# Kernel tuning notes

Hardware: AMD Instinct MI355X
Metric: run time of the kernel (lower is better)

The kernel has to match this reference:

```python
import jax, jax.numpy as jnp
import numpy as np

B, S, D, H, FF = 2, 2048, 1024, 16, 4096
DH = D // H
EPS = 1e-5


def rmsnorm(x, g):
    rms = jnp.sqrt(jnp.mean(x * x, axis=-1, keepdims=True) + EPS)
    return x / rms * g


def gelu(x):
    return x * 0.5 * (1.0 + jax.lax.erf(x / np.float32(np.sqrt(2.0))))


def setup_inputs() -> dict:
    key = jax.random.key(0)
    ks = jax.random.split(key, 9)
    sd = np.float32(1.0 / np.sqrt(D))
    sf = np.float32(1.0 / np.sqrt(FF))
    return {
        'x': jax.random.normal(ks[0], (B, S, D), jnp.float32),
        'wq': jax.random.normal(ks[1], (D, D), jnp.float32) * sd,
        'wk': jax.random.normal(ks[2], (D, D), jnp.float32) * sd,
        'wv': jax.random.normal(ks[3], (D, D), jnp.float32) * sd,
        'wo': jax.random.normal(ks[4], (D, D), jnp.float32) * sd,
        'w1': jax.random.normal(ks[5], (FF, D), jnp.float32) * sd,
        'w2': jax.random.normal(ks[6], (D, FF), jnp.float32) * sf,
        'g1': jax.random.uniform(ks[7], (D,), jnp.float32),
        'g2': jax.random.uniform(ks[8], (D,), jnp.float32),
    }


def reference(x, wq, wk, wv, wo, w1, w2, g1, g2):
    b, s, d = x.shape
    h = rmsnorm(x, g1)
    # torch Linear: y = x @ W.T ; split heads -> [b, s, H, DH]
    q = jnp.einsum('bsd,ed->bse', h, wq).reshape(b, s, H, DH)
    k = jnp.einsum('bsd,ed->bse', h, wk).reshape(b, s, H, DH)
    v = jnp.einsum('bsd,ed->bse', h, wv).reshape(b, s, H, DH)
    score = jnp.einsum('bqhd,bkhd->bhqk', q, k) / np.float32(np.sqrt(DH))
    causal = jnp.triu(jnp.ones((s, s), bool), 1)  # strictly upper = masked
    score = score + jnp.where(causal, jnp.float32(-1e9), jnp.float32(0.0))
    attn_w = jax.nn.softmax(score, axis=-1)
    o = jnp.einsum('bhqk,bkhd->bqhd', attn_w, v).reshape(b, s, d)
    attn_out = jnp.einsum('bsd,ed->bse', o, wo)
    x2 = attn_out + x
    h2 = rmsnorm(x2, g2)
    ffn = jnp.einsum('bsf,df->bsd', gelu(jnp.einsum('bsd,fd->bsf', h2, w1)), w2)
    return ffn + x2
```

## Files before the change

### kernel.cpp

```cpp
#include <hip/hip_runtime.h>
#include <cstdint>

#define B_ 2
#define S_ 2048
#define D_ 1024
#define H_ 16
#define DH_ 64
#define FF_ 4096
#define M_TOK (B_ * S_)

typedef __attribute__((ext_vector_type(8))) short short8;
typedef __attribute__((ext_vector_type(4))) float f32x4;
typedef __attribute__((ext_vector_type(4))) unsigned short us4;

typedef unsigned short u16;

#define SCL 0.18033688011112042f

__device__ __forceinline__ float bf2f(u16 u) {
  union { uint32_t u; float f; } x;
  x.u = ((uint32_t)u) << 16;
  return x.f;
}
__device__ __forceinline__ u16 f2bf(float f) {
  union { float f; uint32_t u; } x;
  x.f = f;
  uint32_t r = x.u + 0x7FFFu + ((x.u >> 16) & 1u);
  return (u16)(r >> 16);
}

__device__ __forceinline__ void gl_lds16(const void* g, void* l) {
  __builtin_amdgcn_global_load_lds(
      (const __attribute__((address_space(1))) uint32_t*)(uintptr_t)g,
      (__attribute__((address_space(3))) uint32_t*)(uintptr_t)l, 16, 0, 0);
}

__device__ __forceinline__ float gelu_f(float v) {
  const float y = 0.7978845608f * (v + 0.044715f * v * v * v);
  const float t = exp2f(y * 2.885390082f);
  const float th = 1.0f - 2.0f * __builtin_amdgcn_rcpf(t + 1.0f);
  return 0.5f * v * (1.0f + th);
}

#define MEG 1048576
__global__ __launch_bounds__(256) void cvt_all_k(const float* __restrict__ wq, const float* __restrict__ wk,
                                                 const float* __restrict__ wv, const float* __restrict__ wo,
                                                 const float* __restrict__ w1, const float* __restrict__ w2,
                                                 u16* __restrict__ wqkv, u16* __restrict__ wob,
                                                 u16* __restrict__ w1b, u16* __restrict__ w2b) {
  const int n = (blockIdx.x * 256 + threadIdx.x) * 4;
  const float* src;
  u16* dst;
  int off;
  if (n < 3 * MEG) {
    dst = wqkv; off = n;
    src = (n < MEG) ? wq + n : (n < 2 * MEG ? wk + (n - MEG) : wv + (n - 2 * MEG));
  } else if (n < 4 * MEG) {
    dst = wob; off = n - 3 * MEG; src = wo + off;
  } else if (n < 8 * MEG) {
    dst = w1b; off = n - 4 * MEG; src = w1 + off;
  } else {
    dst = w2b; off = n - 8 * MEG; src = w2 + off;
  }
  const float4 v = *(const float4*)src;
  us4 o;
  o[0] = f2bf(v.x); o[1] = f2bf(v.y); o[2] = f2bf(v.z); o[3] = f2bf(v.w);
  *(us4*)&dst[off] = o;
}

__global__ __launch_bounds__(256) void zero_k(float* __restrict__ Of, float* __restrict__ L) {
  const int i = (blockIdx.x * 256 + threadIdx.x) * 4;
  if (i < 4 * MEG) { *(float4*)&Of[i] = float4{0.f, 0.f, 0.f, 0.f}; }
  else { *(float4*)&L[i - 4 * MEG] = float4{0.f, 0.f, 0.f, 0.f}; }
}

__global__ __launch_bounds__(256) void norm_o_k(const float* __restrict__ Of, const float* __restrict__ L,
                                                u16* __restrict__ O) {
  const int row = blockIdx.x;
  const int tid = threadIdx.x;
  const int col = tid * 4;
  const int hh = col >> 6;
  const float lv = L[(size_t)((row >> 11) * 16 + hh) * 2048 + (row & 2047)];
  const float inv = 1.0f / lv;
  const float4 v = *(const float4*)&Of[(size_t)row * D_ + col];
  us4 o;
  o[0] = f2bf(v.x * inv); o[1] = f2bf(v.y * inv);
  o[2] = f2bf(v.z * inv); o[3] = f2bf(v.w * inv);
  *(us4*)&O[(size_t)row * D_ + col] = o;
}

__global__ __launch_bounds__(256) void rmsnorm_k(const float* __restrict__ X,
                                                 const float* __restrict__ G,
                                                 u16* __restrict__ Hout) {
  const int row = blockIdx.x;
  const int tid = threadIdx.x;
  const float4 xx = *(const float4*)&X[(size_t)row * D_ + tid * 4];
  float v[4] = {xx.x, xx.y, xx.z, xx.w};
  float s = 0.f;
#pragma unroll
  for (int i = 0; i < 4; ++i) s += v[i] * v[i];
#pragma unroll
  for (int d = 1; d < 64; d <<= 1) s += __shfl_xor(s, d);
  __shared__ float red[4];
  if ((tid & 63) == 0) red[tid >> 6] = s;
  __syncthreads();
  s = red[0] + red[1] + red[2] + red[3];
  const float scale = rsqrtf(s * (1.0f / (float)D_) + 1e-5f);
  const float4 gg = *(const float4*)&G[tid * 4];
  us4 o;
  o[0] = f2bf(v[0] * scale * gg.x);
  o[1] = f2bf(v[1] * scale * gg.y);
  o[2] = f2bf(v[2] * scale * gg.z);
  o[3] = f2bf(v[3] * scale * gg.w);
  *(us4*)&Hout[(size_t)row * D_ + tid * 4] = o;
}

__global__ __launch_bounds__(256) void rmsnorm_wo_k(const u16* __restrict__ P0, const u16* __restrict__ P1,
                                                    const float* __restrict__ X, const float* __restrict__ G,
                                                    float* __restrict__ X2, u16* __restrict__ Hout) {
  const int row = blockIdx.x;
  const int tid = threadIdx.x;
  const size_t off = (size_t)row * D_ + tid * 4;
  const us4 p0 = *(const us4*)&P0[off];
  const us4 p1 = *(const us4*)&P1[off];
  const float4 xx = *(const float4*)&X[off];
  float v[4];
  v[0] = bf2f(p0[0]) + bf2f(p1[0]) + xx.x;
  v[1] = bf2f(p0[1]) + bf2f(p1[1]) + xx.y;
  v[2] = bf2f(p0[2]) + bf2f(p1[2]) + xx.z;
  v[3] = bf2f(p0[3]) + bf2f(p1[3]) + xx.w;
  *(float4*)&X2[off] = float4{v[0], v[1], v[2], v[3]};
  float s = 0.f;
#pragma unroll
  for (int i = 0; i < 4; ++i) s += v[i] * v[i];
#pragma unroll
  for (int d = 1; d < 64; d <<= 1) s += __shfl_xor(s, d);
  __shared__ float red[4];
  if ((tid & 63) == 0) red[tid >> 6] = s;
  __syncthreads();
  s = red[0] + red[1] + red[2] + red[3];
  const float scale = rsqrtf(s * (1.0f / (float)D_) + 1e-5f);
  const float4 gg = *(const float4*)&G[tid * 4];
  us4 o;
  o[0] = f2bf(v[0] * scale * gg.x);
  o[1] = f2bf(v[1] * scale * gg.y);
  o[2] = f2bf(v[2] * scale * gg.z);
  o[3] = f2bf(v[3] * scale * gg.w);
  *(us4*)&Hout[off] = o;
}

__global__ __launch_bounds__(256) void ffn2_red_k(const u16* __restrict__ Q0, const u16* __restrict__ Q1,
                                                  float* __restrict__ OUT) {
  const int i = (blockIdx.x * 256 + threadIdx.x) * 4;
  const us4 a = *(const us4*)&Q0[i];
  const us4 b = *(const us4*)&Q1[i];
  const float4 c = *(const float4*)&OUT[i];
  *(float4*)&OUT[i] = float4{bf2f(a[0]) + bf2f(b[0]) + c.x, bf2f(a[1]) + bf2f(b[1]) + c.y,
                             bf2f(a[2]) + bf2f(b[2]) + c.z, bf2f(a[3]) + bf2f(b[3]) + c.w};
}

template <int MODE>
__global__ __launch_bounds__(256) void gemm_bt_k(const u16* __restrict__ A,
                                                 const u16* __restrict__ W,
                                                 u16* __restrict__ C0, u16* __restrict__ C1,
                                                 u16* __restrict__ C2, int N, int K) {
  __shared__ alignas(16) u16 As[128 * 32];
  __shared__ alignas(16) u16 Bs[128 * 32];
  const int tid = threadIdx.x;
  const int wv = tid >> 6, lane = tid & 63;
  const int r = lane & 15, quad = lane >> 4;
  const int nx = gridDim.x;
  const int nwg = nx * gridDim.y;
  const int orig = blockIdx.x + nx * blockIdx.y;
  const int id = (orig & 7) * (nwg >> 3) + (orig >> 3);
  const int bn = (id % nx) * 128;
  const int bm = (id / nx) * 128;
  const int row0 = (wv >> 1) * 64, col0 = (wv & 1) * 64;

  f32x4 acc[4][4] = {};

  int srow[2], sg[2];
#pragma unroll
  for (int jj = 0; jj < 2; ++jj) {
    const int c = wv * 128 + jj * 64 + lane;
    srow[jj] = c >> 2;
    sg[jj] = (c & 3) ^ ((srow[jj] >> 1) & 3);
  }

  for (int k0 = 0; k0 < K; k0 += 32) {
#pragma unroll
    for (int jj = 0; jj < 2; ++jj) {
      const int l0 = (wv * 128 + jj * 64) * 8;
      gl_lds16(&A[(size_t)(bm + srow[jj]) * K + k0 + sg[jj] * 8], &As[l0]);
      gl_lds16(&W[(size_t)(bn + srow[jj]) * K + k0 + sg[jj] * 8], &Bs[l0]);
    }
    __syncthreads();
    short8 af[4], bf[4];
#pragma unroll
    for (int mt = 0; mt < 4; ++mt) {
      const int mr = row0 + mt * 16 + r;
      af[mt] = *(const short8*)&As[mr * 32 + (quad ^ ((mr >> 1) & 3)) * 8];
    }
#pragma unroll
    for (int nt = 0; nt < 4; ++nt) {
      const int nr = col0 + nt * 16 + r;
      bf[nt] = *(const short8*)&Bs[nr * 32 + (quad ^ ((nr >> 1) & 3)) * 8];
    }
#pragma unroll
    for (int mt = 0; mt < 4; ++mt)
#pragma unroll
      for (int nt = 0; nt < 4; ++nt)
        acc[mt][nt] = __builtin_amdgcn_mfma_f32_16x16x32_bf16(af[mt], bf[nt], acc[mt][nt], 0, 0, 0);
    __syncthreads();
  }

  if constexpr (MODE == 2) {
#pragma unroll
    for (int mt = 0; mt < 4; ++mt)
#pragma unroll
      for (int nt = 0; nt < 4; ++nt)
#pragma unroll
        for (int i = 0; i < 4; ++i) {
          const int grow = bm + row0 + mt * 16 + quad * 4 + i;
          const int gcol = bn + col0 + nt * 16 + r;
          C0[(size_t)grow * N + gcol] = f2bf(gelu_f(acc[mt][nt][i]));
        }
  } else {
#pragma unroll
    for (int mt = 0; mt < 4; ++mt) {
      const int grow0 = bm + row0 + mt * 16 + quad * 4;
#pragma unroll
      for (int nt = 0; nt < 4; ++nt) {
        const int gcol = bn + col0 + nt * 16 + r;
        if (gcol < 2048) {
          u16* dst = (gcol < 1024) ? C0 : C1;
          const float sc = (gcol < 1024) ? SCL : 1.0f;
          const int cc = gcol & 1023;
#pragma unroll
          for (int i = 0; i < 4; ++i)
            dst[(size_t)(grow0 + i) * 1024 + cc] = f2bf(acc[mt][nt][i] * sc);
        } else {
          const int vcol = gcol - 2048;
          us4 o;
#pragma unroll
          for (int i = 0; i < 4; ++i) o[i] = f2bf(acc[mt][nt][i]);
          const size_t addr =
              ((size_t)((grow0 >> 11) * 16 + (vcol >> 6)) * 64 + (vcol & 63)) * 2048 + (grow0 & 2047);
          *(us4*)&C2[addr] = o;
        }
      }
    }
  }
}

__global__ __launch_bounds__(256) void gemm_sk2_k(const u16* __restrict__ A,
                                                  const u16* __restrict__ W,
                                                  u16* __restrict__ P0, u16* __restrict__ P1,
                                                  int N, int K, int KS) {
  __shared__ alignas(16) u16 As[128 * 32];
  __shared__ alignas(16) u16 Bs[128 * 32];
  const int tid = threadIdx.x;
  const int wv = tid >> 6, lane = tid & 63;
  const int r = lane & 15, quad = lane >> 4;
  const int orig = blockIdx.x + 8 * (blockIdx.y + 32 * blockIdx.z);
  const int id = (orig & 7) * 64 + (orig >> 3);
  const int bn = (id & 7) * 128;
  const int bm = ((id >> 3) & 31) * 128;
  const int bz = id >> 8;
  const int row0 = (wv >> 1) * 64, col0 = (wv & 1) * 64;
  const int koff = bz * KS;
  u16* P = bz ? P1 : P0;

  f32x4 acc[4][4] = {};

  int srow[2], sg[2];
#pragma unroll
  for (int jj = 0; jj < 2; ++jj) {
    const int c = wv * 128 + jj * 64 + lane;
    srow[jj] = c >> 2;
    sg[jj] = (c & 3) ^ ((srow[jj] >> 1) & 3);
  }

  for (int k0 = koff; k0 < koff + KS; k0 += 32) {
#pragma unroll
    for (int jj = 0; jj < 2; ++jj) {
      const int l0 = (wv * 128 + jj * 64) * 8;
      gl_lds16(&A[(size_t)(bm + srow[jj]) * K + k0 + sg[jj] * 8], &As[l0]);
      gl_lds16(&W[(size_t)(bn + srow[jj]) * K + k0 + sg[jj] * 8], &Bs[l0]);
    }
    __syncthreads();
    short8 af[4], bf[4];
#pragma unroll
    for (int mt = 0; mt < 4; ++mt) {
      const int mr = row0 + mt * 16 + r;
      af[mt] = *(const short8*)&As[mr * 32 + (quad ^ ((mr >> 1) & 3)) * 8];
    }
#pragma unroll
    for (int nt = 0; nt < 4; ++nt) {
      const int nr = col0 + nt * 16 + r;
      bf[nt] = *(const short8*)&Bs[nr * 32 + (quad ^ ((nr >> 1) & 3)) * 8];
    }
#pragma unroll
    for (int mt = 0; mt < 4; ++mt)
#pragma unroll
      for (int nt = 0; nt < 4; ++nt)
        acc[mt][nt] = __builtin_amdgcn_mfma_f32_16x16x32_bf16(af[mt], bf[nt], acc[mt][nt], 0, 0, 0);
    __syncthreads();
  }

#pragma unroll
  for (int mt = 0; mt < 4; ++mt)
#pragma unroll
    for (int nt = 0; nt < 4; ++nt)
#pragma unroll
      for (int i = 0; i < 4; ++i) {
        const int grow = bm + row0 + mt * 16 + quad * 4 + i;
        const int gcol = bn + col0 + nt * 16 + r;
        P[(size_t)grow * N + gcol] = f2bf(acc[mt][nt][i]);
      }
}

__global__ __launch_bounds__(256, 4) void attn_k(const u16* __restrict__ Q,
                                                 const u16* __restrict__ Kx,
                                                 const u16* __restrict__ VT,
                                                 float* __restrict__ Of, float* __restrict__ L) {
  __shared__ alignas(16) u16 Ks[2][32 * 72];
  __shared__ alignas(16) u16 Vs[2][64 * 40];
  __shared__ alignas(16) u16 Ps[4][32 * 40];

  const int tid = threadIdx.x;
  const int wv = tid >> 6, lane = tid & 63;
  const int r = lane & 15, quad = lane >> 4;

  const int orig = blockIdx.x + 40 * blockIdx.y;
  const int sid = (orig & 7) * 160 + (orig >> 3);
  const int sx = sid % 40;
  const int bh = sid / 40;
  const int b = bh >> 4, hh = bh & 15;

  int id = 39 - sx;
  int bx = 0;
  for (;;) {
    const int nb = (bx >> 2) + 1;
    if (id < nb) break;
    id -= nb;
    ++bx;
  }
  const int c = id;
  const int j0base = c * 512;
  const int niter = (min(bx * 128 + 128, j0base + 512) - j0base) >> 5;

  const int qbase = bx * 128;
  const int m0 = qbase + wv * 32;
  const size_t base = (size_t)b * S_ * D_ + (size_t)hh * DH_;
  const u16* Qb = Q + base;
  const u16* Kb = Kx + base;
  const u16* VTb = VT + (size_t)bh * 64 * 2048;
  u16* Psw = &Ps[wv][0];

  short8 qf[2][2];
#pragma unroll
  for (int f = 0; f < 2; ++f) {
    qf[f][0] = *(const short8*)&Qb[(size_t)(m0 + f * 16 + r) * D_ + quad * 8];
    qf[f][1] = *(const short8*)&Qb[(size_t)(m0 + f * 16 + r) * D_ + 32 + quad * 8];
  }

  short8 onesv;
#pragma unroll
  for (int e = 0; e < 8; ++e) onesv[e] = (short)0x3F80;

  f32x4 oacc[2][4] = {};
  f32x4 lacc[2] = {};

  const int krow = tid >> 3, kg = tid & 7;
  const int vrow = tid >> 2, vg = tid & 3;

  *(short8*)&Ks[0][krow * 72 + kg * 8] = *(const short8*)&Kb[(size_t)(j0base + krow) * D_ + kg * 8];
  {
    const u16* vsrc = &VTb[(size_t)vrow * 2048 + j0base];
    const us4 va = *(const us4*)&vsrc[vg * 4];
    const us4 vb = *(const us4*)&vsrc[vg * 4 + 16];
    short8 o;
    o[0] = va[0]; o[1] = vb[0]; o[2] = va[1]; o[3] = vb[1];
    o[4] = va[2]; o[5] = vb[2]; o[6] = va[3]; o[7] = vb[3];
    *(short8*)&Vs[0][vrow * 40 + vg * 8] = o;
  }

  int cur = 0;
  for (int it = 0; it < niter; ++it) {
    const int j0 = j0base + it * 32;
    __syncthreads();

    if (it + 1 < niter) {
      const int j1 = j0 + 32;
      *(short8*)&Ks[cur ^ 1][krow * 72 + kg * 8] =
          *(const short8*)&Kb[(size_t)(j1 + krow) * D_ + kg * 8];
      const u16* vsrc = &VTb[(size_t)vrow * 2048 + j1];
      const us4 va = *(const us4*)&vsrc[vg * 4];
      const us4 vb = *(const us4*)&vsrc[vg * 4 + 16];
      short8 o;
      o[0] = va[0]; o[1] = vb[0]; o[2] = va[1]; o[3] = vb[1];
      o[4] = va[2]; o[5] = vb[2]; o[6] = va[3]; o[7] = vb[3];
      *(short8*)&Vs[cur ^ 1][vrow * 40 + vg * 8] = o;
    }

    f32x4 z[2][2];
    __builtin_amdgcn_s_setprio(1);
#pragma unroll
    for (int kt = 0; kt < 2; ++kt) {
      const short8 kf0 = *(const short8*)&Ks[cur][(kt * 16 + r) * 72 + quad * 8];
      const short8 kf1 = *(const short8*)&Ks[cur][(kt * 16 + r) * 72 + 32 + quad * 8];
#pragma unroll
      for (int f = 0; f < 2; ++f) {
        f32x4 zz = {};
        zz = __builtin_amdgcn_mfma_f32_16x16x32_bf16(qf[f][0], kf0, zz, 0, 0, 0);
        zz = __builtin_amdgcn_mfma_f32_16x16x32_bf16(qf[f][1], kf1, zz, 0, 0, 0);
        z[f][kt] = zz;
      }
    }
    __builtin_amdgcn_s_setprio(0);

    const bool masked = (j0 + 31 > m0);
#pragma unroll
    for (int f = 0; f < 2; ++f)
#pragma unroll
      for (int i = 0; i < 4; ++i) {
        const int qrow = m0 + f * 16 + quad * 4 + i;
        float v0 = z[f][0][i];
        float v1 = z[f][1][i];
        if (masked) {
          if (j0 + r > qrow) v0 = -128.f;
          if (j0 + 16 + r > qrow) v1 = -128.f;
        }
        const float e0 = exp2f(v0);
        const float e1 = exp2f(v1);
        const uint32_t pk = (uint32_t)f2bf(e0) | ((uint32_t)f2bf(e1) << 16);
        *(uint32_t*)&Psw[(f * 16 + quad * 4 + i) * 40 + r * 2] = pk;
      }

    asm volatile("s_waitcnt lgkmcnt(0)" ::: "memory");

    short8 vf[4];
#pragma unroll
    for (int nt = 0; nt < 4; ++nt)
      vf[nt] = *(const short8*)&Vs[cur][(nt * 16 + r) * 40 + quad * 8];
    __builtin_amdgcn_s_setprio(1);
#pragma unroll
    for (int f = 0; f < 2; ++f) {
      const short8 pf = *(const short8*)&Psw[(f * 16 + r) * 40 + quad * 8];
#pragma unroll
      for (int nt = 0; nt < 4; ++nt)
        oacc[f][nt] = __builtin_amdgcn_mfma_f32_16x16x32_bf16(pf, vf[nt], oacc[f][nt], 0, 0, 0);
      lacc[f] = __builtin_amdgcn_mfma_f32_16x16x32_bf16(pf, onesv, lacc[f], 0, 0, 0);
    }
    __builtin_amdgcn_s_setprio(0);

    cur ^= 1;
  }

#pragma unroll
  for (int f = 0; f < 2; ++f) {
#pragma unroll
    for (int i = 0; i < 4; ++i) {
      const int qrow = m0 + f * 16 + quad * 4 + i;
#pragma unroll
      for (int nt = 0; nt < 4; ++nt)
        atomicAdd(&Of[base + (size_t)qrow * D_ + nt * 16 + r], oacc[f][nt][i]);
      if (r == 0) atomicAdd(&L[(size_t)bh * 2048 + qrow], lacc[f][i]);
    }
  }
}

extern "C" void kernel_launch(void* const* d_in, const int* in_sizes, int n_in,
                              void* d_out, int out_size, void* d_ws, size_t ws_size,
                              hipStream_t stream) {
  (void)in_sizes; (void)n_in; (void)out_size; (void)ws_size;
  const float* x   = (const float*)d_in[0];
  const float* wq  = (const float*)d_in[1];
  const float* wk  = (const float*)d_in[2];
  const float* wvp = (const float*)d_in[3];
  const float* wo  = (const float*)d_in[4];
  const float* w1  = (const float*)d_in[5];
  const float* w2  = (const float*)d_in[6];
  const float* g1  = (const float*)d_in[7];
  const float* g2  = (const float*)d_in[8];
  float* out = (float*)d_out;

  u16* ws = (u16*)d_ws;
  const size_t TD = (size_t)M_TOK * D_;
  u16* h    = ws;
  u16* q    = ws + 1 * TD;
  u16* k    = ws + 2 * TD;
  u16* vt   = ws + 3 * TD;
  u16* h2   = ws + 4 * TD;
  float* l  = (float*)(ws + 4 * TD);
  u16* o    = h;
  u16* t    = ws;
  u16* P0   = q;
  u16* P1   = k;
  u16* Q0   = h2;
  u16* wqkv = ws + 5 * TD;
  u16* wob  = wqkv + 3 * MEG;
  u16* w1b  = wob + 1 * MEG;
  u16* w2b  = w1b + 4 * MEG;
  u16* Q1   = w2b + 4 * MEG;

  const dim3 blk(256);

  cvt_all_k<<<12288, blk, 0, stream>>>(wq, wk, wvp, wo, w1, w2, wqkv, wob, w1b, w2b);
  zero_k<<<(4 * MEG + 65536) / 1024, blk, 0, stream>>>(out, l);
  rmsnorm_k<<<M_TOK, blk, 0, stream>>>(x, g1, h);
  gemm_bt_k<4><<<dim3(24, 32), blk, 0, stream>>>(h, wqkv, q, k, vt, 3072, 1024);
  attn_k<<<dim3(40, 32), blk, 0, stream>>>(q, k, vt, out, l);
  norm_o_k<<<M_TOK, blk, 0, stream>>>(out, l, o);
  gemm_sk2_k<<<dim3(8, 32, 2), blk, 0, stream>>>(o, wob, P0, P1, 1024, 1024, 512);
  rmsnorm_wo_k<<<M_TOK, blk, 0, stream>>>(P0, P1, x, g2, out, h2);
  gemm_bt_k<2><<<dim3(32, 32), blk, 0, stream>>>(h2, w1b, t, nullptr, nullptr, 4096, 1024);
  gemm_sk2_k<<<dim3(8, 32, 2), blk, 0, stream>>>(t, w2b, Q0, Q1, 1024, 4096, 2048);
  ffn2_red_k<<<4096, blk, 0, stream>>>(Q0, Q1, out);
}
```

Baseline: 378.7 us.

## Raise split-K from two to four ways and simplify attention V and P staging

The Wo and FFN2 GEMMs now split K four ways instead of two. This doubles the number of workgroups from 512 to 1024 to improve CU occupancy, and the partial sums are reduced in the rmsnorm and final reduction kernels. Two extra partial buffers are carved from workspace regions that are dead at that point, including the converted wqkv and w1 weight areas. The attention kernel drops the interleaved V-load shuffle and the packed P store in favour of natural column order, and relaxes its launch bounds from 4 to 2 waves per SIMD. The cost is extra partial-buffer traffic and a possible occupancy change in attention.

```diff
diff --git a/kernel.cpp b/kernel.cpp
--- a/kernel.cpp
+++ b/kernel.cpp
@@ -116,6 +116,7 @@
 }
 
 __global__ __launch_bounds__(256) void rmsnorm_wo_k(const u16* __restrict__ P0, const u16* __restrict__ P1,
+                                                    const u16* __restrict__ P2, const u16* __restrict__ P3,
                                                     const float* __restrict__ X, const float* __restrict__ G,
                                                     float* __restrict__ X2, u16* __restrict__ Hout) {
   const int row = blockIdx.x;
@@ -123,12 +124,14 @@
   const size_t off = (size_t)row * D_ + tid * 4;
   const us4 p0 = *(const us4*)&P0[off];
   const us4 p1 = *(const us4*)&P1[off];
+  const us4 p2 = *(const us4*)&P2[off];
+  const us4 p3 = *(const us4*)&P3[off];
   const float4 xx = *(const float4*)&X[off];
   float v[4];
-  v[0] = bf2f(p0[0]) + bf2f(p1[0]) + xx.x;
-  v[1] = bf2f(p0[1]) + bf2f(p1[1]) + xx.y;
-  v[2] = bf2f(p0[2]) + bf2f(p1[2]) + xx.z;
-  v[3] = bf2f(p0[3]) + bf2f(p1[3]) + xx.w;
+  v[0] = (bf2f(p0[0]) + bf2f(p1[0])) + (bf2f(p2[0]) + bf2f(p3[0])) + xx.x;
+  v[1] = (bf2f(p0[1]) + bf2f(p1[1])) + (bf2f(p2[1]) + bf2f(p3[1])) + xx.y;
+  v[2] = (bf2f(p0[2]) + bf2f(p1[2])) + (bf2f(p2[2]) + bf2f(p3[2])) + xx.z;
+  v[3] = (bf2f(p0[3]) + bf2f(p1[3])) + (bf2f(p2[3]) + bf2f(p3[3])) + xx.w;
   *(float4*)&X2[off] = float4{v[0], v[1], v[2], v[3]};
   float s = 0.f;
 #pragma unroll
@@ -150,13 +153,19 @@
 }
 
 __global__ __launch_bounds__(256) void ffn2_red_k(const u16* __restrict__ Q0, const u16* __restrict__ Q1,
+                                                  const u16* __restrict__ Q2, const u16* __restrict__ Q3,
                                                   float* __restrict__ OUT) {
   const int i = (blockIdx.x * 256 + threadIdx.x) * 4;
   const us4 a = *(const us4*)&Q0[i];
   const us4 b = *(const us4*)&Q1[i];
+  const us4 c2 = *(const us4*)&Q2[i];
+  const us4 d = *(const us4*)&Q3[i];
   const float4 c = *(const float4*)&OUT[i];
-  *(float4*)&OUT[i] = float4{bf2f(a[0]) + bf2f(b[0]) + c.x, bf2f(a[1]) + bf2f(b[1]) + c.y,
-                             bf2f(a[2]) + bf2f(b[2]) + c.z, bf2f(a[3]) + bf2f(b[3]) + c.w};
+  *(float4*)&OUT[i] =
+      float4{(bf2f(a[0]) + bf2f(b[0])) + (bf2f(c2[0]) + bf2f(d[0])) + c.x,
+             (bf2f(a[1]) + bf2f(b[1])) + (bf2f(c2[1]) + bf2f(d[1])) + c.y,
+             (bf2f(a[2]) + bf2f(b[2])) + (bf2f(c2[2]) + bf2f(d[2])) + c.z,
+             (bf2f(a[3]) + bf2f(b[3])) + (bf2f(c2[3]) + bf2f(d[3])) + c.w};
 }
 
 template <int MODE>
@@ -253,9 +262,10 @@
   }
 }
 
-__global__ __launch_bounds__(256) void gemm_sk2_k(const u16* __restrict__ A,
+__global__ __launch_bounds__(256) void gemm_sk4_k(const u16* __restrict__ A,
                                                   const u16* __restrict__ W,
                                                   u16* __restrict__ P0, u16* __restrict__ P1,
+                                                  u16* __restrict__ P2, u16* __restrict__ P3,
                                                   int N, int K, int KS) {
   __shared__ alignas(16) u16 As[128 * 32];
   __shared__ alignas(16) u16 Bs[128 * 32];
@@ -263,13 +273,13 @@
   const int wv = tid >> 6, lane = tid & 63;
   const int r = lane & 15, quad = lane >> 4;
   const int orig = blockIdx.x + 8 * (blockIdx.y + 32 * blockIdx.z);
-  const int id = (orig & 7) * 64 + (orig >> 3);
+  const int id = (orig & 7) * 128 + (orig >> 3);
   const int bn = (id & 7) * 128;
   const int bm = ((id >> 3) & 31) * 128;
   const int bz = id >> 8;
   const int row0 = (wv >> 1) * 64, col0 = (wv & 1) * 64;
   const int koff = bz * KS;
-  u16* P = bz ? P1 : P0;
+  u16* P = (bz == 0) ? P0 : (bz == 1) ? P1 : (bz == 2) ? P2 : P3;
 
   f32x4 acc[4][4] = {};
 
@@ -320,7 +330,7 @@
       }
 }
 
-__global__ __launch_bounds__(256, 4) void attn_k(const u16* __restrict__ Q,
+__global__ __launch_bounds__(256, 2) void attn_k(const u16* __restrict__ Q,
                                                  const u16* __restrict__ Kx,
                                                  const u16* __restrict__ VT,
                                                  float* __restrict__ Of, float* __restrict__ L) {
@@ -376,15 +386,7 @@
   const int vrow = tid >> 2, vg = tid & 3;
 
   *(short8*)&Ks[0][krow * 72 + kg * 8] = *(const short8*)&Kb[(size_t)(j0base + krow) * D_ + kg * 8];
-  {
-    const u16* vsrc = &VTb[(size_t)vrow * 2048 + j0base];
-    const us4 va = *(const us4*)&vsrc[vg * 4];
-    const us4 vb = *(const us4*)&vsrc[vg * 4 + 16];
-    short8 o;
-    o[0] = va[0]; o[1] = vb[0]; o[2] = va[1]; o[3] = vb[1];
-    o[4] = va[2]; o[5] = vb[2]; o[6] = va[3]; o[7] = vb[3];
-    *(short8*)&Vs[0][vrow * 40 + vg * 8] = o;
-  }
+  *(short8*)&Vs[0][vrow * 40 + vg * 8] = *(const short8*)&VTb[(size_t)vrow * 2048 + j0base + vg * 8];
 
   int cur = 0;
   for (int it = 0; it < niter; ++it) {
@@ -395,13 +397,8 @@
       const int j1 = j0 + 32;
       *(short8*)&Ks[cur ^ 1][krow * 72 + kg * 8] =
           *(const short8*)&Kb[(size_t)(j1 + krow) * D_ + kg * 8];
-      const u16* vsrc = &VTb[(size_t)vrow * 2048 + j1];
-      const us4 va = *(const us4*)&vsrc[vg * 4];
-      const us4 vb = *(const us4*)&vsrc[vg * 4 + 16];
-      short8 o;
-      o[0] = va[0]; o[1] = vb[0]; o[2] = va[1]; o[3] = vb[1];
-      o[4] = va[2]; o[5] = vb[2]; o[6] = va[3]; o[7] = vb[3];
-      *(short8*)&Vs[cur ^ 1][vrow * 40 + vg * 8] = o;
+      *(short8*)&Vs[cur ^ 1][vrow * 40 + vg * 8] =
+          *(const short8*)&VTb[(size_t)vrow * 2048 + j1 + vg * 8];
     }
 
     f32x4 z[2][2];
@@ -432,10 +429,8 @@
           if (j0 + r > qrow) v0 = -128.f;
           if (j0 + 16 + r > qrow) v1 = -128.f;
         }
-        const float e0 = exp2f(v0);
-        const float e1 = exp2f(v1);
-        const uint32_t pk = (uint32_t)f2bf(e0) | ((uint32_t)f2bf(e1) << 16);
-        *(uint32_t*)&Psw[(f * 16 + quad * 4 + i) * 40 + r * 2] = pk;
+        Psw[(f * 16 + quad * 4 + i) * 40 + r] = f2bf(exp2f(v0));
+        Psw[(f * 16 + quad * 4 + i) * 40 + 16 + r] = f2bf(exp2f(v1));
       }
 
     asm volatile("s_waitcnt lgkmcnt(0)" ::: "memory");
@@ -498,12 +493,16 @@
   u16* t    = ws;
   u16* P0   = q;
   u16* P1   = k;
-  u16* Q0   = h2;
+  u16* P2   = vt;
+  u16* P3   = h2;
   u16* wqkv = ws + 5 * TD;
   u16* wob  = wqkv + 3 * MEG;
   u16* w1b  = wob + 1 * MEG;
   u16* w2b  = w1b + 4 * MEG;
-  u16* Q1   = w2b + 4 * MEG;
+  u16* Q0   = h2;
+  u16* Q1   = wqkv;
+  u16* Q2   = w1b;
+  u16* Q3   = w2b + 4 * MEG;
 
   const dim3 blk(256);
 
@@ -513,9 +512,9 @@
   gemm_bt_k<4><<<dim3(24, 32), blk, 0, stream>>>(h, wqkv, q, k, vt, 3072, 1024);
   attn_k<<<dim3(40, 32), blk, 0, stream>>>(q, k, vt, out, l);
   norm_o_k<<<M_TOK, blk, 0, stream>>>(out, l, o);
-  gemm_sk2_k<<<dim3(8, 32, 2), blk, 0, stream>>>(o, wob, P0, P1, 1024, 1024, 512);
-  rmsnorm_wo_k<<<M_TOK, blk, 0, stream>>>(P0, P1, x, g2, out, h2);
+  gemm_sk4_k<<<dim3(8, 32, 4), blk, 0, stream>>>(o, wob, P0, P1, P2, P3, 1024, 1024, 256);
+  rmsnorm_wo_k<<<M_TOK, blk, 0, stream>>>(P0, P1, P2, P3, x, g2, out, h2);
   gemm_bt_k<2><<<dim3(32, 32), blk, 0, stream>>>(h2, w1b, t, nullptr, nullptr, 4096, 1024);
-  gemm_sk2_k<<<dim3(8, 32, 2), blk, 0, stream>>>(t, w2b, Q0, Q1, 1024, 4096, 2048);
-  ffn2_red_k<<<4096, blk, 0, stream>>>(Q0, Q1, out);
-}
+  gemm_sk4_k<<<dim3(8, 32, 4), blk, 0, stream>>>(t, w2b, Q0, Q1, Q2, Q3, 1024, 4096, 1024);
+  ffn2_red_k<<<4096, blk, 0, stream>>>(Q0, Q1, Q2, Q3, out);
+}
```

Result: no change. 384.6 us (+1.6%).
